# Kernel optimization log

Measured on AMD Instinct MI355X. Metric: run time of the kernel, lower is better.

## Reference

```python
import jax, jax.numpy as jnp
import numpy as np

DIM = 1024
NUM_HEADS = 16
HEAD_DIM = DIM // NUM_HEADS


def setup_inputs() -> dict:
    key = jax.random.key(0)
    k1, k2, k3 = jax.random.split(key, 3)
    scale = 1.0 / np.sqrt(DIM)
    x = jax.random.normal(k1, (4, 2048, DIM), dtype=jnp.float32)
    w_qkv = jax.random.normal(k2, (DIM, 3 * DIM), dtype=jnp.float32) * scale
    b_qkv = jnp.zeros((3 * DIM,), dtype=jnp.float32)
    w_out = jax.random.normal(k3, (DIM, DIM), dtype=jnp.float32) * scale
    b_out = jnp.zeros((DIM,), dtype=jnp.float32)
    return {"x": x, "w_qkv": w_qkv, "b_qkv": b_qkv, "w_out": w_out, "b_out": b_out}


def reference(x, w_qkv, b_qkv, w_out, b_out):
    B, S, D = x.shape
    H, Hd = NUM_HEADS, HEAD_DIM
    qkv = x @ w_qkv + b_qkv  # [B,S,3D]
    q, k, v = jnp.split(qkv, 3, axis=-1)
    # [B,H,S,Hd]
    q = q.reshape(B, S, H, Hd).transpose(0, 2, 1, 3)
    k = k.reshape(B, S, H, Hd).transpose(0, 2, 1, 3)
    v = v.reshape(B, S, H, Hd).transpose(0, 2, 1, 3)
    scores = jnp.einsum('bhqd,bhkd->bhqk', q, k) / np.sqrt(Hd).astype(np.float32)
    causal = jnp.triu(jnp.ones((S, S), dtype=bool), k=1)  # True above diagonal -> masked
    scores = jnp.where(causal[None, None], -jnp.inf, scores)
    scores = scores - jnp.max(scores, axis=-1, keepdims=True)
    attn = jax.nn.softmax(scores, axis=-1)
    out = jnp.einsum('bhqk,bhkd->bhqd', attn, v)  # [B,H,S,Hd]
    out = out.transpose(0, 2, 1, 3).reshape(B, S, D)
    return out @ w_out + b_out
```

## Files before the change

### kernel.cpp

```cpp
#include <hip/hip_runtime.h>

typedef unsigned short u16;
typedef unsigned int u32;
using f32x4 = __attribute__((ext_vector_type(4))) float;
using f32x16 = __attribute__((ext_vector_type(16))) float;
using u32x4 = __attribute__((ext_vector_type(4))) u32;
typedef u32x4 __attribute__((may_alias)) u32x4a;
typedef uint2 __attribute__((may_alias)) uint2a;
using bf16x8 = __attribute__((ext_vector_type(8))) __bf16;

#define SEQ 2048

__device__ __forceinline__ u16 f2bf(float f) {
  union { float f; u32 u; } c; c.f = f;
  return (u16)((c.u + 0x7fffu + ((c.u >> 16) & 1u)) >> 16);
}
__device__ __forceinline__ float bf2f(u16 h) {
  union { u32 u; float f; } c; c.u = ((u32)h) << 16;
  return c.f;
}
__device__ __forceinline__ bf16x8 ld16(const u16* p) {
  return __builtin_bit_cast(bf16x8, *(const u32x4a*)p);
}
__device__ __forceinline__ f32x4 mfma16(bf16x8 a, bf16x8 b, f32x4 c) {
  return __builtin_amdgcn_mfma_f32_16x16x32_bf16(a, b, c, 0, 0, 0);
}
__device__ __forceinline__ f32x16 mfma32(bf16x8 a, bf16x8 b, f32x16 c) {
  return __builtin_amdgcn_mfma_f32_32x32x16_bf16(a, b, c, 0, 0, 0);
}
__device__ __forceinline__ void gload_lds16(const u16* g, u16* l) {
  __builtin_amdgcn_global_load_lds(
      (const __attribute__((address_space(1))) void*)g,
      (__attribute__((address_space(3))) void*)l, 16, 0, 0);
}
__device__ __forceinline__ u32 cvtpk(float lo, float hi) {
  u32 r;
  asm("v_cvt_pk_bf16_f32 %0, %1, %2" : "=v"(r) : "v"(lo), "v"(hi));
  return r;
}
__device__ __forceinline__ void plane32_swap(u32& a, u32& b) {
  asm("v_permlane32_swap_b32 %0, %1" : "+v"(a), "+v"(b));
}

__global__ void detect_dtype(const u16* __restrict__ x, int* __restrict__ flag) {
  if (threadIdx.x == 0) {
    int cnt = 0;
    for (int i = 0; i < 32; ++i) {
      const int e = (x[2 * i] >> 7) & 0xFF;
      cnt += (e >= 100 && e <= 140) ? 1 : 0;
    }
    *flag = (cnt >= 20) ? 1 : 0;
  }
}


__global__ __launch_bounds__(256)
void cvt_x(const void* __restrict__ in, u16* __restrict__ out,
           const int* __restrict__ flag, size_t eoff4) {
  const size_t i = (size_t)blockIdx.x * 256 + threadIdx.x;
  if (*flag) {
    ((uint2*)out)[i] = ((const uint2*)in)[eoff4 + i];
  } else {
    const float4 v = ((const float4*)in)[eoff4 + i];
    uint2 ov;
    ov.x = (u32)f2bf(v.x) | ((u32)f2bf(v.y) << 16);
    ov.y = (u32)f2bf(v.z) | ((u32)f2bf(v.w) << 16);
    ((uint2*)out)[i] = ov;
  }
}

__global__ __launch_bounds__(256)
void cvt_bias(const void* __restrict__ in, float* __restrict__ out, int n,
              const int* __restrict__ flag) {
  const int i = blockIdx.x * 256 + threadIdx.x;
  if (i >= n) return;
  out[i] = (*flag) ? bf2f(((const u16*)in)[i]) : ((const float*)in)[i];
}

__global__ __launch_bounds__(256)
void transpose_w(const void* __restrict__ in, u16* __restrict__ out, int K, int N,
                 const int* __restrict__ flag) {
  __shared__ float t[64][65];
  const int tid = threadIdx.x;
  const int r = tid >> 4, c4 = tid & 15;
  const int n0 = blockIdx.x << 6, k0 = blockIdx.y << 6;
  const int fl = *flag;
#pragma unroll
  for (int i = 0; i < 4; ++i) {
    const int kk = r + i * 16;
    const size_t base = (size_t)(k0 + kk) * N + n0 + c4 * 4;
    if (fl) {
      const uint2 raw = *(const uint2*)((const u16*)in + base);
      t[kk][c4 * 4 + 0] = bf2f((u16)(raw.x & 0xFFFF));
      t[kk][c4 * 4 + 1] = bf2f((u16)(raw.x >> 16));
      t[kk][c4 * 4 + 2] = bf2f((u16)(raw.y & 0xFFFF));
      t[kk][c4 * 4 + 3] = bf2f((u16)(raw.y >> 16));
    } else {
      const float4 v = *(const float4*)((const float*)in + base);
      t[kk][c4 * 4 + 0] = v.x; t[kk][c4 * 4 + 1] = v.y;
      t[kk][c4 * 4 + 2] = v.z; t[kk][c4 * 4 + 3] = v.w;
    }
  }
  __syncthreads();
#pragma unroll
  for (int i = 0; i < 4; ++i) {
    const int nn = r + i * 16;
    uint2 ov;
    ov.x = (u32)f2bf(t[c4 * 4 + 0][nn]) | ((u32)f2bf(t[c4 * 4 + 1][nn]) << 16);
    ov.y = (u32)f2bf(t[c4 * 4 + 2][nn]) | ((u32)f2bf(t[c4 * 4 + 3][nn]) << 16);
    *(uint2*)&out[(size_t)(n0 + nn) * K + k0 + c4 * 4] = ov;
  }
}

__global__ __launch_bounds__(256)
void transpose_v(const u16* __restrict__ qkv, u16* __restrict__ vt) {
  __shared__ __align__(16) u16 t[64][72];
  const int h = blockIdx.x, s0 = blockIdx.y << 6, b = blockIdx.z;
  const int tid = threadIdx.x;
  const int r = tid >> 2, g = tid & 3;
  const u16* src = &qkv[(size_t)(b * SEQ + s0 + r) * 3072 + 2048 + h * 64 + g * 16];
  *(u32x4a*)&t[r][g * 16]     = *(const u32x4a*)src;
  *(u32x4a*)&t[r][g * 16 + 8] = *(const u32x4a*)(src + 8);
  __syncthreads();
  union { u16 s[16]; u32x4 v[2]; } u;
#pragma unroll
  for (int e = 0; e < 16; ++e) u.s[e] = t[g * 16 + e][r];
  u16* dst = &vt[(size_t)((b * 16 + h) * 64 + r) * 2048 + s0 + g * 16];
  *(u32x4a*)dst = u.v[0];
  *(u32x4a*)(dst + 8) = u.v[1];
}

template <bool BF16_OUT>
__global__ __launch_bounds__(512, 2)
void gemm_bt(const u16* __restrict__ A, const u16* __restrict__ BT,
             const float* __restrict__ bias, void* __restrict__ Cv,
             int M, int N, int K) {
  constexpr int BK = 32;
  __shared__ __align__(16) u16 ring[4][12288];
  const int tid = threadIdx.x;
  const int wid = tid >> 6, lane = tid & 63;
  const int quad = lane >> 4, l16 = lane & 15;

  const int nbx = gridDim.x, nwg = nbx * gridDim.y;
  int bid = blockIdx.y * nbx + blockIdx.x;
  if ((nwg & 7) == 0) bid = (bid & 7) * (nwg >> 3) + (bid >> 3);
  const int tile_n = (bid % nbx) << 7;
  const int tile_m = (bid / nbx) << 8;

  const int wmR = (wid >> 1) << 6;
  const int wnR = (wid & 1) << 6;

  const int G0 = wid * 64 + lane;
  const int rA0 = G0 >> 2;
  const int sA0 = (((G0 & 3) ^ ((rA0 & 3) ^ ((rA0 >> 2) & 3)))) * 8;
  const int G1 = G0 + 512;
  const int rA1 = G1 >> 2;
  const int sA1 = (((G1 & 3) ^ ((rA1 & 3) ^ ((rA1 >> 2) & 3)))) * 8;
  const u16* const pA0 = A + (size_t)(tile_m + rA0) * K + sA0;
  const u16* const pA1 = A + (size_t)(tile_m + rA1) * K + sA1;
  const u16* const pB0 = BT + (size_t)(tile_n + rA0) * K + sA0;
  const int dst0 = wid * 512;
  const int dst1 = 4096 + wid * 512;
  const int dstB = 8192 + wid * 512;

  const int swl = (l16 & 3) ^ ((l16 >> 2) & 3);
  const int cA = (quad ^ swl) * 8;

  const int nk = K >> 5;
  f32x4 acc[4][4] = {};

  auto STAGE = [&](int kt) {
    u16* bp = ring[kt & 3];
    const size_t ko = (size_t)kt * BK;
    gload_lds16(pA0 + ko, bp + dst0);
    gload_lds16(pA1 + ko, bp + dst1);
    gload_lds16(pB0 + ko, bp + dstB);
  };

  STAGE(0);
  if (nk > 1) STAGE(1);
  if (nk > 2) STAGE(2);

  for (int kt = 0; kt < nk; ++kt) {
    asm volatile("s_waitcnt vmcnt(6)" ::: "memory");
    __builtin_amdgcn_sched_barrier(0);
    __builtin_amdgcn_s_barrier();
    __builtin_amdgcn_sched_barrier(0);
    if (kt + 3 < nk) STAGE(kt + 3);
    const u16* bp = ring[kt & 3];
    bf16x8 af[4], bfr[4];
#pragma unroll
    for (int i = 0; i < 4; ++i)
      af[i] = ld16(&bp[(wmR + i * 16 + l16) * BK + cA]);
#pragma unroll
    for (int j = 0; j < 4; ++j)
      bfr[j] = ld16(&bp[8192 + (wnR + j * 16 + l16) * BK + cA]);
    asm volatile("s_waitcnt lgkmcnt(0)" ::: "memory");
    __builtin_amdgcn_sched_barrier(0);
    __builtin_amdgcn_s_setprio(1);
#pragma unroll
    for (int i = 0; i < 4; ++i)
#pragma unroll
      for (int j = 0; j < 4; ++j) acc[i][j] = mfma16(af[i], bfr[j], acc[i][j]);
    __builtin_amdgcn_s_setprio(0);
  }

#pragma unroll
  for (int j = 0; j < 4; ++j) {
    const int cg = tile_n + wnR + j * 16 + l16;
    const float bv = bias[cg];
#pragma unroll
    for (int i = 0; i < 4; ++i) {
      const int rg = tile_m + wmR + i * 16 + quad * 4;
#pragma unroll
      for (int r = 0; r < 4; ++r) {
        const float v = acc[i][j][r] + bv;
        if constexpr (BF16_OUT)
          ((u16*)Cv)[(size_t)(rg + r) * N + cg] = f2bf(v);
        else
          ((float*)Cv)[(size_t)(rg + r) * N + cg] = v;
      }
    }
  }
}

__global__ __launch_bounds__(256, 2)
void attn_fwd(const u16* __restrict__ qkv, const u16* __restrict__ vt,
              u16* __restrict__ aout) {
  const int h = blockIdx.x, b = blockIdx.z;
  const int tid = threadIdx.x, wid = tid >> 6, lane = tid & 63;
  const int l31 = lane & 31, hi = lane >> 5;
  __shared__ __align__(16) u16 lK[2][4096];
  __shared__ __align__(16) u16 lV[2][4096];

  const int G0 = wid * 64 + lane, G1 = G0 + 256;
  const int r0 = G0 >> 3, c0 = ((G0 & 7) ^ (r0 & 7)) * 8;
  const int r1 = G1 >> 3, c1 = ((G1 & 7) ^ (r1 & 7)) * 8;
  const int db0 = wid * 512, db1 = 2048 + wid * 512;

  const u16* const kg = qkv + (size_t)(b * SEQ) * 3072 + 1024 + h * 64;
  const u16* const vg = vt + (size_t)((b * 16 + h) * 64) * 2048;

  constexpr float SC = 0.1803368801f;
  constexpr float THR = 44.3614196f;

  u32x4 onesu;
  onesu[0] = onesu[1] = onesu[2] = onesu[3] = 0x3F803F80u;
  const bf16x8 ones = __builtin_bit_cast(bf16x8, onesu);

  const int sx = l31 & 7;
  int cur = 0;

#pragma unroll 1
  for (int pass = 0; pass < 2; ++pass) {
    const int qt = pass ? (int)blockIdx.y : 15 - (int)blockIdx.y;
    const int q0w = qt * 128 + wid * 32;
    const int qrow = q0w + l31;
    bf16x8 qf[4];
#pragma unroll
    for (int d = 0; d < 4; ++d)
      qf[d] = ld16(&qkv[(size_t)(b * SEQ + qrow) * 3072 + h * 64 + d * 16 + hi * 8]);
    f32x16 o0 = {}, o1 = {}, lacc = {};
    float m_r = -1e30f, ms = -1.8e29f;

    gload_lds16(kg + (size_t)r0 * 3072 + c0, &lK[cur][db0]);
    gload_lds16(kg + (size_t)r1 * 3072 + c1, &lK[cur][db1]);
    gload_lds16(vg + (size_t)r0 * 2048 + c0, &lV[cur][db0]);
    gload_lds16(vg + (size_t)r1 * 2048 + c1, &lV[cur][db1]);
    __syncthreads();

    const int last = 2 * qt + 1;
    for (int kt = 0; kt <= last; ++kt) {
      const int kb = kt * 64;
      if (kt < last) {
        const int kn = kb + 64;
        gload_lds16(kg + (size_t)(kn + r0) * 3072 + c0, &lK[cur ^ 1][db0]);
        gload_lds16(kg + (size_t)(kn + r1) * 3072 + c1, &lK[cur ^ 1][db1]);
        gload_lds16(vg + (size_t)r0 * 2048 + kn + c0, &lV[cur ^ 1][db0]);
        gload_lds16(vg + (size_t)r1 * 2048 + kn + c1, &lV[cur ^ 1][db1]);
      }
      if (kb <= q0w + 31) {
        const u16* const lKc = lK[cur];
        const u16* const lVc = lV[cur];
        f32x16 s0 = {}, s1 = {};
#pragma unroll
        for (int d = 0; d < 4; ++d) {
          const bf16x8 kf = ld16(&lKc[l31 * 64 + (((d * 2 + hi) ^ sx)) * 8]);
          s0 = mfma32(kf, qf[d], s0);
        }
#pragma unroll
        for (int d = 0; d < 4; ++d) {
          const bf16x8 kf = ld16(&lKc[(32 + l31) * 64 + (((d * 2 + hi) ^ sx)) * 8]);
          s1 = mfma32(kf, qf[d], s1);
        }
        bf16x8 vf[2][2][2];
#pragma unroll
        for (int kh = 0; kh < 2; ++kh)
#pragma unroll
          for (int j = 0; j < 2; ++j)
#pragma unroll
            for (int dh = 0; dh < 2; ++dh)
              vf[kh][j][dh] = ld16(
                  &lVc[(dh * 32 + l31) * 64 + (((kh * 4 + j * 2 + hi) ^ sx)) * 8]);
        if (kb + 63 > q0w) {
          const int rel = qrow - kb - 4 * hi;
#pragma unroll
          for (int i = 0; i < 16; ++i) {
            const int kc = (i & 3) + 8 * (i >> 2);
            if (kc > rel) s0[i] = -1e30f;
            if (kc + 32 > rel) s1[i] = -1e30f;
          }
        }
        float pm = fmaxf(fmaxf(s0[0], s0[1]), s0[2]);
        pm = fmaxf(fmaxf(pm, s0[3]), s0[4]);
        pm = fmaxf(fmaxf(pm, s0[5]), s0[6]);
        pm = fmaxf(fmaxf(pm, s0[7]), s0[8]);
        pm = fmaxf(fmaxf(pm, s0[9]), s0[10]);
        pm = fmaxf(fmaxf(pm, s0[11]), s0[12]);
        pm = fmaxf(fmaxf(pm, s0[13]), s0[14]);
        pm = fmaxf(fmaxf(pm, s0[15]), s1[0]);
        pm = fmaxf(fmaxf(pm, s1[1]), s1[2]);
        pm = fmaxf(fmaxf(pm, s1[3]), s1[4]);
        pm = fmaxf(fmaxf(pm, s1[5]), s1[6]);
        pm = fmaxf(fmaxf(pm, s1[7]), s1[8]);
        pm = fmaxf(fmaxf(pm, s1[9]), s1[10]);
        pm = fmaxf(fmaxf(pm, s1[11]), s1[12]);
        pm = fmaxf(fmaxf(pm, s1[13]), s1[14]);
        pm = fmaxf(pm, s1[15]);
        if (__any(pm > m_r + THR)) {
          const float mm = fmaxf(pm, __shfl_xor(pm, 32));
          const float mn = fmaxf(m_r, mm);
          const float al = exp2f((m_r - mn) * SC);
#pragma unroll
          for (int i = 0; i < 16; ++i) {
            o0[i] *= al; o1[i] *= al; lacc[i] *= al;
          }
          m_r = mn;
          ms = mn * SC;
        }
#pragma unroll
        for (int i = 0; i < 16; ++i) {
          s0[i] = exp2f(fmaf(s0[i], SC, -ms));
          s1[i] = exp2f(fmaf(s1[i], SC, -ms));
        }
        u32 t0 = cvtpk(s0[0], s0[1]), t1 = cvtpk(s0[2], s0[3]);
        u32 t2 = cvtpk(s0[4], s0[5]), t3 = cvtpk(s0[6], s0[7]);
        u32 t4 = cvtpk(s0[8], s0[9]), t5 = cvtpk(s0[10], s0[11]);
        u32 t6 = cvtpk(s0[12], s0[13]), t7 = cvtpk(s0[14], s0[15]);
        plane32_swap(t0, t2); plane32_swap(t1, t3);
        plane32_swap(t4, t6); plane32_swap(t5, t7);
        u32x4 w00, w01;
        w00[0] = t0; w00[1] = t1; w00[2] = t2; w00[3] = t3;
        w01[0] = t4; w01[1] = t5; w01[2] = t6; w01[3] = t7;
        u32 u0 = cvtpk(s1[0], s1[1]), u1 = cvtpk(s1[2], s1[3]);
        u32 u2 = cvtpk(s1[4], s1[5]), u3 = cvtpk(s1[6], s1[7]);
        u32 u4 = cvtpk(s1[8], s1[9]), u5 = cvtpk(s1[10], s1[11]);
        u32 u6 = cvtpk(s1[12], s1[13]), u7 = cvtpk(s1[14], s1[15]);
        plane32_swap(u0, u2); plane32_swap(u1, u3);
        plane32_swap(u4, u6); plane32_swap(u5, u7);
        u32x4 w10, w11;
        w10[0] = u0; w10[1] = u1; w10[2] = u2; w10[3] = u3;
        w11[0] = u4; w11[1] = u5; w11[2] = u6; w11[3] = u7;
        const bf16x8 pb00 = __builtin_bit_cast(bf16x8, w00);
        const bf16x8 pb01 = __builtin_bit_cast(bf16x8, w01);
        const bf16x8 pb10 = __builtin_bit_cast(bf16x8, w10);
        const bf16x8 pb11 = __builtin_bit_cast(bf16x8, w11);
        o0 = mfma32(vf[0][0][0], pb00, o0);
        o1 = mfma32(vf[0][0][1], pb00, o1);
        lacc = mfma32(ones, pb00, lacc);
        o0 = mfma32(vf[0][1][0], pb01, o0);
        o1 = mfma32(vf[0][1][1], pb01, o1);
        lacc = mfma32(ones, pb01, lacc);
        o0 = mfma32(vf[1][0][0], pb10, o0);
        o1 = mfma32(vf[1][0][1], pb10, o1);
        lacc = mfma32(ones, pb10, lacc);
        o0 = mfma32(vf[1][1][0], pb11, o0);
        o1 = mfma32(vf[1][1][1], pb11, o1);
        lacc = mfma32(ones, pb11, lacc);
      }
      __syncthreads();
      cur ^= 1;
    }
    const float inv = 1.0f / lacc[0];
    u16* const orow = &aout[(size_t)(b * SEQ + qrow) * 1024 + h * 64];
#pragma unroll
    for (int t = 0; t < 4; ++t) {
      const int d0 = 8 * t + 4 * hi;
      uint2a wv;
      wv.x = cvtpk(o0[4 * t] * inv, o0[4 * t + 1] * inv);
      wv.y = cvtpk(o0[4 * t + 2] * inv, o0[4 * t + 3] * inv);
      *(uint2a*)&orow[d0] = wv;
      wv.x = cvtpk(o1[4 * t] * inv, o1[4 * t + 1] * inv);
      wv.y = cvtpk(o1[4 * t + 2] * inv, o1[4 * t + 3] * inv);
      *(uint2a*)&orow[32 + d0] = wv;
    }
  }
}

extern "C" void kernel_launch(void* const* d_in, const int* in_sizes, int n_in,
                              void* d_out, int out_size, void* d_ws, size_t ws_size,
                              hipStream_t stream) {
  const void* x     = d_in[0];
  const void* w_qkv = d_in[1];
  const void* b_qkv = d_in[2];
  const void* w_out = d_in[3];
  const void* b_out = d_in[4];
  float* out = (float*)d_out;

  float* bqf   = (float*)d_ws;
  float* bof   = bqf + 3072;
  int*   flag  = (int*)(bof + 1024);
  u16*   wqkvT = (u16*)(flag + 4);
  u16*   woutT = wqkvT + (size_t)3072 * 1024;
  u16*   xb    = woutT + (size_t)1024 * 1024;

  detect_dtype<<<dim3(1), dim3(64), 0, stream>>>((const u16*)x, flag);
  cvt_bias<<<dim3(12), dim3(256), 0, stream>>>(b_qkv, bqf, 3072, flag);
  cvt_bias<<<dim3(4), dim3(256), 0, stream>>>(b_out, bof, 1024, flag);
  transpose_w<<<dim3(48, 16), dim3(256), 0, stream>>>(w_qkv, wqkvT, 1024, 3072, flag);
  transpose_w<<<dim3(16, 16), dim3(256), 0, stream>>>(w_out, woutT, 1024, 1024, flag);

  const size_t FULL_WS = 92291088;
  if (ws_size >= FULL_WS) {
    u16* qkv = xb  + (size_t)8192 * 1024;
    u16* vt  = qkv + (size_t)8192 * 3072;
    cvt_x<<<dim3(8192), dim3(256), 0, stream>>>(x, xb, flag, 0);
    gemm_bt<true ><<<dim3(24, 32), dim3(512), 0, stream>>>(xb, wqkvT, bqf, qkv,
                                                           8192, 3072, 1024);
    transpose_v<<<dim3(16, 32, 4), dim3(256), 0, stream>>>(qkv, vt);
    attn_fwd<<<dim3(16, 8, 4), dim3(256), 0, stream>>>(qkv, vt, xb);
    gemm_bt<false><<<dim3(8, 32), dim3(512), 0, stream>>>(xb, woutT, bof, out,
                                                          8192, 1024, 1024);
  } else {
    u16* qkvb = xb   + (size_t)2048 * 1024;
    u16* vtb  = qkvb + (size_t)2048 * 3072;
    for (int b = 0; b < 4; ++b) {
      const size_t eoff4 = (size_t)b * 2048 * 1024 / 4;
      cvt_x<<<dim3(2048), dim3(256), 0, stream>>>(x, xb, flag, eoff4);
      gemm_bt<true ><<<dim3(24, 8), dim3(512), 0, stream>>>(xb, wqkvT, bqf, qkvb,
                                                            2048, 3072, 1024);
      transpose_v<<<dim3(16, 32, 1), dim3(256), 0, stream>>>(qkvb, vtb);
      attn_fwd<<<dim3(16, 8, 1), dim3(256), 0, stream>>>(qkvb, vtb, xb);
      gemm_bt<false><<<dim3(8, 8), dim3(512), 0, stream>>>(
          xb, woutT, bof, out + (size_t)b * 2048 * 1024, 2048, 1024, 1024);
    }
  }
}
```

Before: 299.1 us.

## Use 4-stage LDS ring with explicit vmcnt waits in attention kernel

Replaces the double-buffered K/V shared memory with a 4-slot ring, prefetching three tiles ahead. Waits use explicit s_waitcnt vmcnt counts and a single barrier per iteration instead of a trailing __syncthreads. K fragments are batched before the MFMAs, and MFMA sections get raised wave priority via s_setprio. This aims to hide global-load latency better, at the cost of doubling LDS use (64KB per block), which may cut occupancy from the 2 blocks/CU launch bound. The hand-written vmcnt counts also rely on no other outstanding vector-memory ops.

```diff
diff --git a/kernel.cpp b/kernel.cpp
--- a/kernel.cpp
+++ b/kernel.cpp
@@ -230,8 +230,7 @@
   const int h = blockIdx.x, b = blockIdx.z;
   const int tid = threadIdx.x, wid = tid >> 6, lane = tid & 63;
   const int l31 = lane & 31, hi = lane >> 5;
-  __shared__ __align__(16) u16 lK[2][4096];
-  __shared__ __align__(16) u16 lV[2][4096];
+  __shared__ __align__(16) u16 ring[4][8192];
 
   const int G0 = wid * 64 + lane, G1 = G0 + 256;
   const int r0 = G0 >> 3, c0 = ((G0 & 7) ^ (r0 & 7)) * 8;
@@ -249,7 +248,15 @@
   const bf16x8 ones = __builtin_bit_cast(bf16x8, onesu);
 
   const int sx = l31 & 7;
-  int cur = 0;
+
+  auto STAGE = [&](int kt) {
+    u16* bp = ring[kt & 3];
+    const int kb = kt * 64;
+    gload_lds16(kg + (size_t)(kb + r0) * 3072 + c0, bp + db0);
+    gload_lds16(kg + (size_t)(kb + r1) * 3072 + c1, bp + db1);
+    gload_lds16(vg + (size_t)r0 * 2048 + kb + c0, bp + 4096 + db0);
+    gload_lds16(vg + (size_t)r1 * 2048 + kb + c1, bp + 4096 + db1);
+  };
 
 #pragma unroll 1
   for (int pass = 0; pass < 2; ++pass) {
@@ -263,36 +270,39 @@
     f32x16 o0 = {}, o1 = {}, lacc = {};
     float m_r = -1e30f, ms = -1.8e29f;
 
-    gload_lds16(kg + (size_t)r0 * 3072 + c0, &lK[cur][db0]);
-    gload_lds16(kg + (size_t)r1 * 3072 + c1, &lK[cur][db1]);
-    gload_lds16(vg + (size_t)r0 * 2048 + c0, &lV[cur][db0]);
-    gload_lds16(vg + (size_t)r1 * 2048 + c1, &lV[cur][db1]);
+    const int last = 2 * qt + 1;
     __syncthreads();
-
-    const int last = 2 * qt + 1;
+    STAGE(0);
+    if (last >= 1) STAGE(1);
+    if (last >= 2) STAGE(2);
+
+#pragma unroll 1
     for (int kt = 0; kt <= last; ++kt) {
+      const int rem = last - kt;
+      if (rem >= 2)      asm volatile("s_waitcnt vmcnt(8)" ::: "memory");
+      else if (rem == 1) asm volatile("s_waitcnt vmcnt(4)" ::: "memory");
+      else               asm volatile("s_waitcnt vmcnt(0)" ::: "memory");
+      __builtin_amdgcn_sched_barrier(0);
+      __builtin_amdgcn_s_barrier();
+      __builtin_amdgcn_sched_barrier(0);
+      if (kt + 3 <= last) STAGE(kt + 3);
       const int kb = kt * 64;
-      if (kt < last) {
-        const int kn = kb + 64;
-        gload_lds16(kg + (size_t)(kn + r0) * 3072 + c0, &lK[cur ^ 1][db0]);
-        gload_lds16(kg + (size_t)(kn + r1) * 3072 + c1, &lK[cur ^ 1][db1]);
-        gload_lds16(vg + (size_t)r0 * 2048 + kn + c0, &lV[cur ^ 1][db0]);
-        gload_lds16(vg + (size_t)r1 * 2048 + kn + c1, &lV[cur ^ 1][db1]);
-      }
       if (kb <= q0w + 31) {
-        const u16* const lKc = lK[cur];
-        const u16* const lVc = lV[cur];
+        const u16* const lKc = ring[kt & 3];
+        const u16* const lVc = ring[kt & 3] + 4096;
         f32x16 s0 = {}, s1 = {};
+        bf16x8 kf0[4], kf1[4];
 #pragma unroll
         for (int d = 0; d < 4; ++d) {
-          const bf16x8 kf = ld16(&lKc[l31 * 64 + (((d * 2 + hi) ^ sx)) * 8]);
-          s0 = mfma32(kf, qf[d], s0);
+          kf0[d] = ld16(&lKc[l31 * 64 + (((d * 2 + hi) ^ sx)) * 8]);
+          kf1[d] = ld16(&lKc[(32 + l31) * 64 + (((d * 2 + hi) ^ sx)) * 8]);
         }
-#pragma unroll
-        for (int d = 0; d < 4; ++d) {
-          const bf16x8 kf = ld16(&lKc[(32 + l31) * 64 + (((d * 2 + hi) ^ sx)) * 8]);
-          s1 = mfma32(kf, qf[d], s1);
-        }
+        __builtin_amdgcn_s_setprio(1);
+#pragma unroll
+        for (int d = 0; d < 4; ++d) s0 = mfma32(kf0[d], qf[d], s0);
+#pragma unroll
+        for (int d = 0; d < 4; ++d) s1 = mfma32(kf1[d], qf[d], s1);
+        __builtin_amdgcn_s_setprio(0);
         bf16x8 vf[2][2][2];
 #pragma unroll
         for (int kh = 0; kh < 2; ++kh)
@@ -365,6 +375,7 @@
         const bf16x8 pb01 = __builtin_bit_cast(bf16x8, w01);
         const bf16x8 pb10 = __builtin_bit_cast(bf16x8, w10);
         const bf16x8 pb11 = __builtin_bit_cast(bf16x8, w11);
+        __builtin_amdgcn_s_setprio(1);
         o0 = mfma32(vf[0][0][0], pb00, o0);
         o1 = mfma32(vf[0][0][1], pb00, o1);
         lacc = mfma32(ones, pb00, lacc);
@@ -377,9 +388,8 @@
         o0 = mfma32(vf[1][1][0], pb11, o0);
         o1 = mfma32(vf[1][1][1], pb11, o1);
         lacc = mfma32(ones, pb11, lacc);
+        __builtin_amdgcn_s_setprio(0);
       }
-      __syncthreads();
-      cur ^= 1;
     }
     const float inv = 1.0f / lacc[0];
     u16* const orow = &aout[(size_t)(b * SEQ + qrow) * 1024 + h * 64];
```

Measured after the change: 295.5 us. No clear change (-1.2%).
